# Kernel optimization log

Hardware: AMD Instinct MI355X
Metric: run time of the kernel (lower is better)

The kernel has to match this reference:

```python
import jax, jax.numpy as jnp
import numpy as np

N = 32768
NIN = 12
NC = 16
HID = 512
K = 8
B = 3.0
L = 8
D_HALF = NIN // 2                      # 6
DIN = D_HALF + NC                      # conditioner input
DOUT = (3 * K - 1) * (NIN - D_HALF)    # conditioner output
MIN_W = 1e-3
MIN_H = 1e-3
MIN_D = 1e-3
DERIV_CONST = float(np.log(np.exp(1.0 - MIN_D) - 1.0))  # softplus^{-1}(1-min_d)


def setup_inputs() -> dict:
    key = jax.random.key(0)
    ks = jax.random.split(key, 12)
    z = jax.random.normal(ks[0], (N, NIN), dtype=jnp.float32)
    c = jax.random.normal(ks[1], (N, NC), dtype=jnp.float32)

    def lin(k, fan_in, shape):
        bound = 1.0 / np.sqrt(fan_in)
        return jax.random.uniform(k, shape, jnp.float32, -bound, bound)

    W0 = lin(ks[2], DIN, (L, DIN, HID)); b0 = lin(ks[3], DIN, (L, HID))
    W1 = lin(ks[4], HID, (L, HID, HID)); b1 = lin(ks[5], HID, (L, HID))
    W2 = lin(ks[6], HID, (L, HID, HID)); b2 = lin(ks[7], HID, (L, HID))
    W3 = lin(ks[8], HID, (L, HID, DOUT)); b3 = lin(ks[9], HID, (L, DOUT))

    rng = np.random.default_rng(0)
    perms = jnp.asarray(np.stack([rng.permutation(NIN) for _ in range(L - 1)]),
                        dtype=jnp.int32)  # [L-1, NIN]
    return dict(z=z, c=c, W0=W0, b0=b0, W1=W1, b1=b1, W2=W2, b2=b2,
                W3=W3, b3=b3, perms=perms)


def _rqs(x, uw, uh, ud):
    """Unconstrained rational-quadratic spline (forward).
    x: [N, d2]; uw/uh: [N, d2, K]; ud: [N, d2, K+1] (already edge-padded)."""
    widths = jax.nn.softmax(uw, axis=-1)
    widths = MIN_W + (1.0 - MIN_W * K) * widths
    cw = jnp.cumsum(widths, axis=-1)
    cw = jnp.concatenate([jnp.zeros_like(cw[..., :1]), cw], axis=-1)
    cw = 2.0 * B * cw - B
    cw = cw.at[..., 0].set(-B).at[..., -1].set(B)
    w = cw[..., 1:] - cw[..., :-1]

    heights = jax.nn.softmax(uh, axis=-1)
    heights = MIN_H + (1.0 - MIN_H * K) * heights
    ch = jnp.cumsum(heights, axis=-1)
    ch = jnp.concatenate([jnp.zeros_like(ch[..., :1]), ch], axis=-1)
    ch = 2.0 * B * ch - B
    ch = ch.at[..., 0].set(-B).at[..., -1].set(B)
    h = ch[..., 1:] - ch[..., :-1]

    d = MIN_D + jax.nn.softplus(ud)  # [N, d2, K+1]

    xc = jnp.clip(x, -B, B)  # tails are handled by mask below
    # searchsorted: eps added only to the last knot for the search itself
    cw_search = cw.at[..., -1].add(1e-6)
    idx = jnp.clip(jnp.sum((xc[..., None] >= cw_search).astype(jnp.int32),
                           axis=-1) - 1, 0, K - 1)  # [N, d2]

    def g(a):
        return jnp.take_along_axis(a, idx[..., None], axis=-1)[..., 0]

    icw, iw = g(cw), g(w)
    ich, ih = g(ch), g(h)
    idelta = g(h / w)
    id0 = g(d)
    id1 = g(d[..., 1:])

    theta = (xc - icw) / iw
    t1m = theta * (1.0 - theta)
    num = ih * (idelta * theta**2 + id0 * t1m)
    den = idelta + (id0 + id1 - 2.0 * idelta) * t1m
    out = ich + num / den
    dnum = idelta**2 * (id1 * theta**2 + 2.0 * idelta * t1m
                        + id0 * (1.0 - theta)**2)
    lad = jnp.log(dnum) - 2.0 * jnp.log(den)

    inside = (x >= -B) & (x <= B)
    return jnp.where(inside, out, x), jnp.where(inside, lad, 0.0)


def _flow(z, c, W0, b0, W1, b1, W2, b2, W3, b3, perms):
    x = z
    total_ld = jnp.zeros(z.shape[0], dtype=z.dtype)
    for i in range(L):
        x1, x2 = x[:, :D_HALF], x[:, D_HALF:]
        inp = jnp.concatenate([x1, c], axis=-1)
        h0 = jax.nn.elu(inp @ W0[i] + b0[i])
        h1 = jax.nn.elu(h0 @ W1[i] + b1[i])
        h2 = jax.nn.elu(h1 @ W2[i] + b2[i])
        out = (h2 @ W3[i] + b3[i]).reshape(-1, NIN - D_HALF, 3 * K - 1)
        uw, uh, ud = out[..., :K], out[..., K:2 * K], out[..., 2 * K:]
        ud = jnp.pad(ud, ((0, 0), (0, 0), (1, 1)),
                     constant_values=DERIV_CONST)
        x2n, ld = _rqs(x2, uw, uh, ud)
        total_ld = total_ld + jnp.sum(ld, axis=-1)
        x = jnp.concatenate([x1, x2n], axis=-1)
        if i < L - 1:
            x = x[:, perms[i]]
    return x, total_ld


def reference(z, c, W0, b0, W1, b1, W2, b2, W3, b3, perms):
    return _flow(z, c, W0, b0, W1, b1, W2, b2, W3, b3, perms)
```

## Files before the change

### kernel.cpp

```cpp
#include <hip/hip_runtime.h>
#include <hip/hip_fp16.h>

#define NROWS   32768
#define MT      64
#define NTH     512
#define HS      520
#define OS      148
#define BND     3.0f

typedef _Float16 half_t;
typedef __attribute__((ext_vector_type(8))) _Float16 f16x8;
typedef __attribute__((ext_vector_type(4))) _Float16 f16x4;
typedef __attribute__((ext_vector_type(4))) float    f32x4;


__global__ void pack_frag(const float* __restrict__ src, half_t* __restrict__ dst,
                          int K, int Nn, int NT, int KS) {
  int l = blockIdx.z;
  int frag = blockIdx.x * 4 + (threadIdx.x >> 6);
  int lane = threadIdx.x & 63;
  int NF = NT * KS;
  if (frag >= NF) return;
  int nt = frag / KS, ks = frag - nt * KS;
  int n = nt * 16 + (lane & 15);
  int kb = ks * 32 + (lane >> 4) * 8;
  f16x8 v;
#pragma unroll
  for (int e = 0; e < 8; e++) {
    int k = kb + e;
    v[e] = (k < K && n < Nn) ? (half_t)src[((size_t)l * K + k) * Nn + n] : (half_t)0.f;
  }
  *(f16x8*)(dst + ((size_t)l * NF + frag) * 512 + lane * 8) = v;
}

__device__ __forceinline__ float elu_f(float v) {
  return v > 0.f ? v : (__expf(v) - 1.f);
}

__device__ __forceinline__ void gemm_elu(
    const half_t* A, int as, int ksteps,
    const half_t* __restrict__ Wf, int KSW,
    const float* __restrict__ bias,
    half_t* dst,
    int w, int lane, int lm, int lk) {
  f32x4 acc[4][4];
#pragma unroll
  for (int i = 0; i < 4; i++)
#pragma unroll
    for (int j = 0; j < 4; j++) acc[i][j] = (f32x4){0.f, 0.f, 0.f, 0.f};

  f16x8 a[2][4], b[4][4];
#pragma unroll
  for (int s = 0; s < 4; s++)
    if (s < ksteps) {
#pragma unroll
      for (int nt = 0; nt < 4; nt++)
        b[s][nt] = *(const f16x8*)(Wf + ((size_t)((w * 4 + nt) * KSW + s)) * 512 + lane * 8);
    }
#pragma unroll
  for (int s = 0; s < 2; s++)
    if (s < ksteps) {
      int ko = s * 32 + lk * 8;
#pragma unroll
      for (int mf = 0; mf < 4; mf++)
        a[s][mf] = *(const f16x8*)(A + (mf * 16 + lm) * as + ko);
    }
#pragma unroll
  for (int ks = 0; ks < ksteps; ks++) {
    const int bs = ks & 3, asx = ks & 1;
#pragma unroll
    for (int nt = 0; nt < 4; nt++)
#pragma unroll
      for (int mf = 0; mf < 4; mf++)
        acc[mf][nt] = __builtin_amdgcn_mfma_f32_16x16x32_f16(b[bs][nt], a[asx][mf], acc[mf][nt], 0, 0, 0);
    if (ks + 4 < ksteps) {
#pragma unroll
      for (int nt = 0; nt < 4; nt++)
        b[bs][nt] = *(const f16x8*)(Wf + ((size_t)((w * 4 + nt) * KSW + ks + 4)) * 512 + lane * 8);
    }
    if (ks + 2 < ksteps) {
      int ko = (ks + 2) * 32 + lk * 8;
#pragma unroll
      for (int mf = 0; mf < 4; mf++)
        a[asx][mf] = *(const f16x8*)(A + (mf * 16 + lm) * as + ko);
    }
  }
#pragma unroll
  for (int nt = 0; nt < 4; nt++) {
    int n0 = w * 64 + nt * 16 + lk * 4;
    f32x4 bv = *(const f32x4*)(bias + n0);
#pragma unroll
    for (int mf = 0; mf < 4; mf++) {
      f16x4 pv;
#pragma unroll
      for (int r = 0; r < 4; r++) pv[r] = (half_t)elu_f(acc[mf][nt][r] + bv[r]);
      *(f16x4*)(dst + (mf * 16 + lm) * HS + n0) = pv;
    }
  }
}

__device__ __forceinline__ void gemm_out(
    const half_t* A,
    const half_t* __restrict__ Wf,
    const float* __restrict__ bias,
    float* outb,
    int w, int lane, int lm, int lk) {
  f32x4 acc[4][2];
#pragma unroll
  for (int i = 0; i < 4; i++)
#pragma unroll
    for (int j = 0; j < 2; j++) acc[i][j] = (f32x4){0.f, 0.f, 0.f, 0.f};
  const bool has2 = (w == 0);

  f16x8 a[2][4], b[4][2];
#pragma unroll
  for (int s = 0; s < 4; s++) {
    b[s][0] = *(const f16x8*)(Wf + ((size_t)(w * 16 + s)) * 512 + lane * 8);
    if (has2) b[s][1] = *(const f16x8*)(Wf + ((size_t)(8 * 16 + s)) * 512 + lane * 8);
  }
#pragma unroll
  for (int s = 0; s < 2; s++) {
    int ko = s * 32 + lk * 8;
#pragma unroll
    for (int mf = 0; mf < 4; mf++)
      a[s][mf] = *(const f16x8*)(A + (mf * 16 + lm) * HS + ko);
  }
#pragma unroll
  for (int ks = 0; ks < 16; ks++) {
    const int bs = ks & 3, asx = ks & 1;
#pragma unroll
    for (int mf = 0; mf < 4; mf++)
      acc[mf][0] = __builtin_amdgcn_mfma_f32_16x16x32_f16(b[bs][0], a[asx][mf], acc[mf][0], 0, 0, 0);
    if (has2)
#pragma unroll
      for (int mf = 0; mf < 4; mf++)
        acc[mf][1] = __builtin_amdgcn_mfma_f32_16x16x32_f16(b[bs][1], a[asx][mf], acc[mf][1], 0, 0, 0);
    if (ks + 4 < 16) {
      b[bs][0] = *(const f16x8*)(Wf + ((size_t)(w * 16 + ks + 4)) * 512 + lane * 8);
      if (has2) b[bs][1] = *(const f16x8*)(Wf + ((size_t)(8 * 16 + ks + 4)) * 512 + lane * 8);
    }
    if (ks + 2 < 16) {
      int ko = (ks + 2) * 32 + lk * 8;
#pragma unroll
      for (int mf = 0; mf < 4; mf++)
        a[asx][mf] = *(const f16x8*)(A + (mf * 16 + lm) * HS + ko);
    }
  }
  {
    int n0 = w * 16 + lk * 4;
    f32x4 bv = *(const f32x4*)(bias + n0);
#pragma unroll
    for (int mf = 0; mf < 4; mf++) {
      f32x4 ov = acc[mf][0] + bv;
      *(f32x4*)(outb + (mf * 16 + lm) * OS + n0) = ov;
    }
  }
  if (has2) {
    int n0 = 128 + lk * 4;
    f32x4 bv;
#pragma unroll
    for (int r = 0; r < 4; r++) bv[r] = (n0 + r < 138) ? bias[n0 + r] : 0.f;
#pragma unroll
    for (int mf = 0; mf < 4; mf++) {
      f32x4 ov = acc[mf][1] + bv;
      *(f32x4*)(outb + (mf * 16 + lm) * OS + n0) = ov;
    }
  }
}

__global__ __launch_bounds__(NTH, 2) __attribute__((amdgpu_waves_per_eu(2, 2)))
void flow_kernel(const float* __restrict__ z, const float* __restrict__ c,
                 const float* __restrict__ b0, const float* __restrict__ b1,
                 const float* __restrict__ b2, const float* __restrict__ b3,
                 const int* __restrict__ perms,
                 const half_t* __restrict__ W0F, const half_t* __restrict__ W1F,
                 const half_t* __restrict__ W2F, const half_t* __restrict__ W3F,
                 float* __restrict__ out) {
  __shared__ half_t hbufA[MT * HS];
  __shared__ __align__(16) char smemB[MT * HS * 2];
  __shared__ half_t inpb[MT * 40];
  __shared__ half_t cbuf[MT * 16];
  __shared__ float xbuf[MT][12];
  __shared__ float ldpart[MT][6];
  __shared__ float ldtot[MT];
  __shared__ int   permbuf[7][12];

  half_t* hbufB  = (half_t*)smemB;
  float*  outbuf = (float*)smemB;

  int tid = threadIdx.x;
  int w = tid >> 6, lane = tid & 63;
  int lm = lane & 15, lk = lane >> 4;
  int row0 = blockIdx.x * MT;

  for (int it = tid; it < MT * 12; it += NTH) xbuf[it / 12][it % 12] = z[(size_t)row0 * 12 + it];
  for (int it = tid; it < MT * 16; it += NTH) cbuf[it] = (half_t)c[(size_t)row0 * 16 + it];
  for (int it = tid; it < 84; it += NTH) permbuf[it / 12][it % 12] = perms[it];
  if (tid < MT) ldtot[tid] = 0.f;
  __syncthreads();

  for (int l = 0; l < 8; l++) {
    for (int it = tid; it < MT * 32; it += NTH) {
      int m = it >> 5, k = it & 31;
      half_t bv;
      if (k < 6)       bv = (half_t)xbuf[m][k];
      else if (k < 22) bv = cbuf[m * 16 + (k - 6)];
      else             bv = (half_t)0.f;
      inpb[m * 40 + k] = bv;
    }
    __syncthreads();
    gemm_elu(inpb, 40, 1,  W0F + (size_t)l * 32 * 512,      1,  b0 + l * 512, hbufA, w, lane, lm, lk);
    __syncthreads();
    gemm_elu(hbufA, HS, 16, W1F + (size_t)l * 512 * 512,   16,  b1 + l * 512, hbufB, w, lane, lm, lk);
    __syncthreads();
    gemm_elu(hbufB, HS, 16, W2F + (size_t)l * 512 * 512,   16,  b2 + l * 512, hbufA, w, lane, lm, lk);
    __syncthreads();
    gemm_out(hbufA, W3F + (size_t)l * 144 * 512, b3 + l * 138, outbuf, w, lane, lm, lk);
    __syncthreads();

    if (tid < MT * 6) {
      int m = tid / 6, j = tid % 6;
      const float* pr = outbuf + m * OS + j * 23;
      float uw[8], uh[8], dd[9];
#pragma unroll
      for (int i = 0; i < 8; i++) uw[i] = pr[i];
#pragma unroll
      for (int i = 0; i < 8; i++) uh[i] = pr[8 + i];
      dd[0] = 1.f; dd[8] = 1.f;
#pragma unroll
      for (int i = 0; i < 7; i++) {
        float u = pr[16 + i];
        float sp = (u > 15.f) ? u : log1pf(__expf(u));
        dd[i + 1] = 0.001f + sp;
      }
      float mw = uw[0];
#pragma unroll
      for (int i = 1; i < 8; i++) mw = fmaxf(mw, uw[i]);
      float ew[8], sw = 0.f;
#pragma unroll
      for (int i = 0; i < 8; i++) { ew[i] = __expf(uw[i] - mw); sw += ew[i]; }
      float invw = 1.f / sw;
      float cw[9]; cw[0] = -BND;
      float a = 0.f;
#pragma unroll
      for (int i = 0; i < 8; i++) { a += 0.001f + 0.992f * ew[i] * invw; cw[i + 1] = 2.f * BND * a - BND; }
      cw[8] = BND;
      float mh = uh[0];
#pragma unroll
      for (int i = 1; i < 8; i++) mh = fmaxf(mh, uh[i]);
      float eh[8], sh = 0.f;
#pragma unroll
      for (int i = 0; i < 8; i++) { eh[i] = __expf(uh[i] - mh); sh += eh[i]; }
      float invh = 1.f / sh;
      float ch[9]; ch[0] = -BND;
      float ah = 0.f;
#pragma unroll
      for (int i = 0; i < 8; i++) { ah += 0.001f + 0.992f * eh[i] * invh; ch[i + 1] = 2.f * BND * ah - BND; }
      ch[8] = BND;

      float x2 = xbuf[m][6 + j];
      float xc = fminf(fmaxf(x2, -BND), BND);
      int cnt = 0;
#pragma unroll
      for (int i = 0; i < 9; i++) {
        float edge = (i == 8) ? (cw[8] + 1e-6f) : cw[i];
        cnt += (xc >= edge) ? 1 : 0;
      }
      int idx = cnt - 1; idx = idx < 0 ? 0 : (idx > 7 ? 7 : idx);
      float icw = cw[0], iw = cw[1] - cw[0], ich = ch[0], ih = ch[1] - ch[0], d0 = dd[0], d1 = dd[1];
#pragma unroll
      for (int i = 0; i < 8; i++) {
        if (idx == i) {
          icw = cw[i]; iw = cw[i + 1] - cw[i];
          ich = ch[i]; ih = ch[i + 1] - ch[i];
          d0 = dd[i]; d1 = dd[i + 1];
        }
      }
      float delta = ih / iw;
      float th  = (xc - icw) / iw;
      float t1m = th * (1.f - th);
      float num = ih * (delta * th * th + d0 * t1m);
      float den = delta + (d0 + d1 - 2.f * delta) * t1m;
      float outv = ich + num / den;
      float dnum = delta * delta * (d1 * th * th + 2.f * delta * t1m + d0 * (1.f - th) * (1.f - th));
      float lad = logf(dnum) - 2.f * logf(den);
      bool inside = (x2 >= -BND) && (x2 <= BND);
      xbuf[m][6 + j] = inside ? outv : x2;
      ldpart[m][j]   = inside ? lad : 0.f;
    }
    __syncthreads();
    if (tid < MT) {
      float s = ldtot[tid];
#pragma unroll
      for (int j = 0; j < 6; j++) s += ldpart[tid][j];
      ldtot[tid] = s;
    }
    if (l < 7) {
      float v0 = xbuf[tid / 12][permbuf[l][tid % 12]];
      float v1 = 0.f;
      int it1 = tid + NTH;
      if (it1 < MT * 12) v1 = xbuf[it1 / 12][permbuf[l][it1 % 12]];
      __syncthreads();
      xbuf[tid / 12][tid % 12] = v0;
      if (it1 < MT * 12) xbuf[it1 / 12][it1 % 12] = v1;
    }
    __syncthreads();
  }

  for (int it = tid; it < MT * 12; it += NTH) out[(size_t)row0 * 12 + it] = xbuf[it / 12][it % 12];
  if (tid < MT) out[(size_t)NROWS * 12 + row0 + tid] = ldtot[tid];
}

extern "C" void kernel_launch(void* const* d_in, const int* in_sizes, int n_in,
                              void* d_out, int out_size, void* d_ws, size_t ws_size,
                              hipStream_t stream) {
  const float* z  = (const float*)d_in[0];
  const float* c  = (const float*)d_in[1];
  const float* W0 = (const float*)d_in[2];
  const float* b0 = (const float*)d_in[3];
  const float* W1 = (const float*)d_in[4];
  const float* b1 = (const float*)d_in[5];
  const float* W2 = (const float*)d_in[6];
  const float* b2 = (const float*)d_in[7];
  const float* W3 = (const float*)d_in[8];
  const float* b3 = (const float*)d_in[9];
  const int* perms = (const int*)d_in[10];

  unsigned short* wsu = (unsigned short*)d_ws;
  half_t* W0F = (half_t*)(wsu + 0);
  half_t* W1F = (half_t*)(wsu + 131072);
  half_t* W2F = (half_t*)(wsu + 2228224);
  half_t* W3F = (half_t*)(wsu + 4325376);

  pack_frag<<<dim3(8,   1, 8), dim3(256), 0, stream>>>(W0, W0F, 22,  512, 32, 1);
  pack_frag<<<dim3(128, 1, 8), dim3(256), 0, stream>>>(W1, W1F, 512, 512, 32, 16);
  pack_frag<<<dim3(128, 1, 8), dim3(256), 0, stream>>>(W2, W2F, 512, 512, 32, 16);
  pack_frag<<<dim3(36,  1, 8), dim3(256), 0, stream>>>(W3, W3F, 512, 138, 9,  16);

  flow_kernel<<<dim3(NROWS / MT), dim3(NTH), 0, stream>>>(
      z, c, b0, b1, b2, b3, perms, W0F, W1F, W2F, W3F, (float*)d_out);
}
```

Before: 547.8 us.

## Prefetch next GEMM's first weight fragments across layer boundaries via register rings

```diff
diff --git a/kernel.cpp b/kernel.cpp
--- a/kernel.cpp
+++ b/kernel.cpp
@@ -37,54 +37,9 @@
   return v > 0.f ? v : (__expf(v) - 1.f);
 }
 
-__device__ __forceinline__ void gemm_elu(
-    const half_t* A, int as, int ksteps,
-    const half_t* __restrict__ Wf, int KSW,
-    const float* __restrict__ bias,
-    half_t* dst,
-    int w, int lane, int lm, int lk) {
-  f32x4 acc[4][4];
-#pragma unroll
-  for (int i = 0; i < 4; i++)
-#pragma unroll
-    for (int j = 0; j < 4; j++) acc[i][j] = (f32x4){0.f, 0.f, 0.f, 0.f};
-
-  f16x8 a[2][4], b[4][4];
-#pragma unroll
-  for (int s = 0; s < 4; s++)
-    if (s < ksteps) {
-#pragma unroll
-      for (int nt = 0; nt < 4; nt++)
-        b[s][nt] = *(const f16x8*)(Wf + ((size_t)((w * 4 + nt) * KSW + s)) * 512 + lane * 8);
-    }
-#pragma unroll
-  for (int s = 0; s < 2; s++)
-    if (s < ksteps) {
-      int ko = s * 32 + lk * 8;
-#pragma unroll
-      for (int mf = 0; mf < 4; mf++)
-        a[s][mf] = *(const f16x8*)(A + (mf * 16 + lm) * as + ko);
-    }
-#pragma unroll
-  for (int ks = 0; ks < ksteps; ks++) {
-    const int bs = ks & 3, asx = ks & 1;
-#pragma unroll
-    for (int nt = 0; nt < 4; nt++)
-#pragma unroll
-      for (int mf = 0; mf < 4; mf++)
-        acc[mf][nt] = __builtin_amdgcn_mfma_f32_16x16x32_f16(b[bs][nt], a[asx][mf], acc[mf][nt], 0, 0, 0);
-    if (ks + 4 < ksteps) {
-#pragma unroll
-      for (int nt = 0; nt < 4; nt++)
-        b[bs][nt] = *(const f16x8*)(Wf + ((size_t)((w * 4 + nt) * KSW + ks + 4)) * 512 + lane * 8);
-    }
-    if (ks + 2 < ksteps) {
-      int ko = (ks + 2) * 32 + lk * 8;
-#pragma unroll
-      for (int mf = 0; mf < 4; mf++)
-        a[asx][mf] = *(const f16x8*)(A + (mf * 16 + lm) * as + ko);
-    }
-  }
+__device__ __forceinline__ void epi_elu(const f32x4 (&acc)[4][4],
+                                        const float* __restrict__ bias,
+                                        half_t* dst, int w, int lm, int lk) {
 #pragma unroll
   for (int nt = 0; nt < 4; nt++) {
     int n0 = w * 64 + nt * 16 + lk * 4;
@@ -99,11 +54,86 @@
   }
 }
 
+__device__ __forceinline__ void gemm0(const half_t* A, const f16x8 (&b0r)[4],
+                                      const float* __restrict__ bias,
+                                      half_t* dst, int w, int lm, int lk) {
+  f32x4 acc[4][4];
+#pragma unroll
+  for (int i = 0; i < 4; i++)
+#pragma unroll
+    for (int j = 0; j < 4; j++) acc[i][j] = (f32x4){0.f, 0.f, 0.f, 0.f};
+  int ko = lk * 8;
+  f16x8 a[4];
+#pragma unroll
+  for (int mf = 0; mf < 4; mf++) a[mf] = *(const f16x8*)(A + (mf * 16 + lm) * 40 + ko);
+#pragma unroll
+  for (int nt = 0; nt < 4; nt++)
+#pragma unroll
+    for (int mf = 0; mf < 4; mf++)
+      acc[mf][nt] = __builtin_amdgcn_mfma_f32_16x16x32_f16(b0r[nt], a[mf], acc[mf][nt], 0, 0, 0);
+  epi_elu(acc, bias, dst, w, lm, lk);
+}
+
+template <bool FILL4>
+__device__ __forceinline__ void gemm512(
+    const half_t* A, const half_t* __restrict__ Wf,
+    const float* __restrict__ bias, half_t* dst,
+    f16x8 (&ring4)[4][4], f16x8 (&ring2)[4][2],
+    const half_t* __restrict__ nxt,
+    int w, int lane, int lm, int lk) {
+  f32x4 acc[4][4];
+#pragma unroll
+  for (int i = 0; i < 4; i++)
+#pragma unroll
+    for (int j = 0; j < 4; j++) acc[i][j] = (f32x4){0.f, 0.f, 0.f, 0.f};
+
+  f16x8 a[2][4];
+#pragma unroll
+  for (int s = 0; s < 2; s++) {
+    int ko = s * 32 + lk * 8;
+#pragma unroll
+    for (int mf = 0; mf < 4; mf++)
+      a[s][mf] = *(const f16x8*)(A + (mf * 16 + lm) * HS + ko);
+  }
+#pragma unroll
+  for (int ks = 0; ks < 16; ks++) {
+    const int sl = ks & 3, asx = ks & 1;
+#pragma unroll
+    for (int nt = 0; nt < 4; nt++)
+#pragma unroll
+      for (int mf = 0; mf < 4; mf++)
+        acc[mf][nt] = __builtin_amdgcn_mfma_f32_16x16x32_f16(ring4[sl][nt], a[asx][mf], acc[mf][nt], 0, 0, 0);
+    if (ks + 4 < 16) {
+#pragma unroll
+      for (int nt = 0; nt < 4; nt++)
+        ring4[sl][nt] = *(const f16x8*)(Wf + ((size_t)((w * 4 + nt) * 16 + ks + 4)) * 512 + lane * 8);
+    } else {
+      int j = ks - 12;
+      if (FILL4) {
+#pragma unroll
+        for (int nt = 0; nt < 4; nt++)
+          ring4[sl][nt] = *(const f16x8*)(nxt + ((size_t)((w * 4 + nt) * 16 + j)) * 512 + lane * 8);
+      } else {
+        ring2[sl][0] = *(const f16x8*)(nxt + ((size_t)(w * 16 + j)) * 512 + lane * 8);
+        if (w == 0)
+          ring2[sl][1] = *(const f16x8*)(nxt + ((size_t)(128 + j)) * 512 + lane * 8);
+      }
+    }
+    if (ks + 2 < 16) {
+      int ko = (ks + 2) * 32 + lk * 8;
+#pragma unroll
+      for (int mf = 0; mf < 4; mf++)
+        a[asx][mf] = *(const f16x8*)(A + (mf * 16 + lm) * HS + ko);
+    }
+  }
+  epi_elu(acc, bias, dst, w, lm, lk);
+}
+
 __device__ __forceinline__ void gemm_out(
-    const half_t* A,
-    const half_t* __restrict__ Wf,
-    const float* __restrict__ bias,
-    float* outb,
+    const half_t* A, const half_t* __restrict__ Wf,
+    const float* __restrict__ bias, float* outb,
+    f16x8 (&ring2)[4][2], f16x8 (&ring4)[4][4],
+    const half_t* __restrict__ nxtW1,
     int w, int lane, int lm, int lk) {
   f32x4 acc[4][2];
 #pragma unroll
@@ -112,12 +142,7 @@
     for (int j = 0; j < 2; j++) acc[i][j] = (f32x4){0.f, 0.f, 0.f, 0.f};
   const bool has2 = (w == 0);
 
-  f16x8 a[2][4], b[4][2];
-#pragma unroll
-  for (int s = 0; s < 4; s++) {
-    b[s][0] = *(const f16x8*)(Wf + ((size_t)(w * 16 + s)) * 512 + lane * 8);
-    if (has2) b[s][1] = *(const f16x8*)(Wf + ((size_t)(8 * 16 + s)) * 512 + lane * 8);
-  }
+  f16x8 a[2][4];
 #pragma unroll
   for (int s = 0; s < 2; s++) {
     int ko = s * 32 + lk * 8;
@@ -127,17 +152,22 @@
   }
 #pragma unroll
   for (int ks = 0; ks < 16; ks++) {
-    const int bs = ks & 3, asx = ks & 1;
+    const int sl = ks & 3, asx = ks & 1;
 #pragma unroll
     for (int mf = 0; mf < 4; mf++)
-      acc[mf][0] = __builtin_amdgcn_mfma_f32_16x16x32_f16(b[bs][0], a[asx][mf], acc[mf][0], 0, 0, 0);
+      acc[mf][0] = __builtin_amdgcn_mfma_f32_16x16x32_f16(ring2[sl][0], a[asx][mf], acc[mf][0], 0, 0, 0);
     if (has2)
 #pragma unroll
       for (int mf = 0; mf < 4; mf++)
-        acc[mf][1] = __builtin_amdgcn_mfma_f32_16x16x32_f16(b[bs][1], a[asx][mf], acc[mf][1], 0, 0, 0);
+        acc[mf][1] = __builtin_amdgcn_mfma_f32_16x16x32_f16(ring2[sl][1], a[asx][mf], acc[mf][1], 0, 0, 0);
     if (ks + 4 < 16) {
-      b[bs][0] = *(const f16x8*)(Wf + ((size_t)(w * 16 + ks + 4)) * 512 + lane * 8);
-      if (has2) b[bs][1] = *(const f16x8*)(Wf + ((size_t)(8 * 16 + ks + 4)) * 512 + lane * 8);
+      ring2[sl][0] = *(const f16x8*)(Wf + ((size_t)(w * 16 + ks + 4)) * 512 + lane * 8);
+      if (has2) ring2[sl][1] = *(const f16x8*)(Wf + ((size_t)(128 + ks + 4)) * 512 + lane * 8);
+    } else {
+      int j = ks - 12;
+#pragma unroll
+      for (int nt = 0; nt < 4; nt++)
+        ring4[sl][nt] = *(const f16x8*)(nxtW1 + ((size_t)((w * 4 + nt) * 16 + j)) * 512 + lane * 8);
     }
     if (ks + 2 < 16) {
       int ko = (ks + 2) * 32 + lk * 8;
@@ -193,6 +223,13 @@
   int lm = lane & 15, lk = lane >> 4;
   int row0 = blockIdx.x * MT;
 
+  f16x8 ring4[4][4], ring2[4][2];
+#pragma unroll
+  for (int s = 0; s < 4; s++)
+#pragma unroll
+    for (int nt = 0; nt < 4; nt++)
+      ring4[s][nt] = *(const f16x8*)(W1F + ((size_t)((w * 4 + nt) * 16 + s)) * 512 + lane * 8);
+
   for (int it = tid; it < MT * 12; it += NTH) xbuf[it / 12][it % 12] = z[(size_t)row0 * 12 + it];
   for (int it = tid; it < MT * 16; it += NTH) cbuf[it] = (half_t)c[(size_t)row0 * 16 + it];
   for (int it = tid; it < 84; it += NTH) permbuf[it / 12][it % 12] = perms[it];
@@ -200,6 +237,13 @@
   __syncthreads();
 
   for (int l = 0; l < 8; l++) {
+    f16x8 b0r[4];
+    {
+      const half_t* W0l = W0F + (size_t)l * 32 * 512;
+#pragma unroll
+      for (int nt = 0; nt < 4; nt++)
+        b0r[nt] = *(const f16x8*)(W0l + ((size_t)(w * 4 + nt)) * 512 + lane * 8);
+    }
     for (int it = tid; it < MT * 32; it += NTH) {
       int m = it >> 5, k = it & 31;
       half_t bv;
@@ -209,13 +253,17 @@
       inpb[m * 40 + k] = bv;
     }
     __syncthreads();
-    gemm_elu(inpb, 40, 1,  W0F + (size_t)l * 32 * 512,      1,  b0 + l * 512, hbufA, w, lane, lm, lk);
-    __syncthreads();
-    gemm_elu(hbufA, HS, 16, W1F + (size_t)l * 512 * 512,   16,  b1 + l * 512, hbufB, w, lane, lm, lk);
-    __syncthreads();
-    gemm_elu(hbufB, HS, 16, W2F + (size_t)l * 512 * 512,   16,  b2 + l * 512, hbufA, w, lane, lm, lk);
-    __syncthreads();
-    gemm_out(hbufA, W3F + (size_t)l * 144 * 512, b3 + l * 138, outbuf, w, lane, lm, lk);
+
+    gemm0(inpb, b0r, b0 + l * 512, hbufA, w, lm, lk);
+    __syncthreads();
+    gemm512<true >(hbufA, W1F + (size_t)l * 512 * 512, b1 + l * 512, hbufB,
+                   ring4, ring2, W2F + (size_t)l * 512 * 512, w, lane, lm, lk);
+    __syncthreads();
+    gemm512<false>(hbufB, W2F + (size_t)l * 512 * 512, b2 + l * 512, hbufA,
+                   ring4, ring2, W3F + (size_t)l * 144 * 512, w, lane, lm, lk);
+    __syncthreads();
+    gemm_out(hbufA, W3F + (size_t)l * 144 * 512, b3 + l * 138, outbuf,
+             ring2, ring4, W1F + (size_t)((l + 1) & 7) * 512 * 512, w, lane, lm, lk);
     __syncthreads();
 
     if (tid < MT * 6) {
```

After: 570.0 us. 4.1% more time.

## Double block to 16 waves and split GEMM N-tiles across more waves

Applied to the files above, without the earlier changes.

```diff
diff --git a/kernel.cpp b/kernel.cpp
--- a/kernel.cpp
+++ b/kernel.cpp
@@ -3,7 +3,7 @@
 
 #define NROWS   32768
 #define MT      64
-#define NTH     512
+#define NTH     1024
 #define HS      520
 #define OS      148
 #define BND     3.0f
@@ -37,57 +37,12 @@
   return v > 0.f ? v : (__expf(v) - 1.f);
 }
 
-__device__ __forceinline__ void gemm_elu(
-    const half_t* A, int as, int ksteps,
-    const half_t* __restrict__ Wf, int KSW,
-    const float* __restrict__ bias,
-    half_t* dst,
-    int w, int lane, int lm, int lk) {
-  f32x4 acc[4][4];
-#pragma unroll
-  for (int i = 0; i < 4; i++)
-#pragma unroll
-    for (int j = 0; j < 4; j++) acc[i][j] = (f32x4){0.f, 0.f, 0.f, 0.f};
-
-  f16x8 a[2][4], b[4][4];
-#pragma unroll
-  for (int s = 0; s < 4; s++)
-    if (s < ksteps) {
-#pragma unroll
-      for (int nt = 0; nt < 4; nt++)
-        b[s][nt] = *(const f16x8*)(Wf + ((size_t)((w * 4 + nt) * KSW + s)) * 512 + lane * 8);
-    }
-#pragma unroll
-  for (int s = 0; s < 2; s++)
-    if (s < ksteps) {
-      int ko = s * 32 + lk * 8;
-#pragma unroll
-      for (int mf = 0; mf < 4; mf++)
-        a[s][mf] = *(const f16x8*)(A + (mf * 16 + lm) * as + ko);
-    }
-#pragma unroll
-  for (int ks = 0; ks < ksteps; ks++) {
-    const int bs = ks & 3, asx = ks & 1;
-#pragma unroll
-    for (int nt = 0; nt < 4; nt++)
-#pragma unroll
-      for (int mf = 0; mf < 4; mf++)
-        acc[mf][nt] = __builtin_amdgcn_mfma_f32_16x16x32_f16(b[bs][nt], a[asx][mf], acc[mf][nt], 0, 0, 0);
-    if (ks + 4 < ksteps) {
-#pragma unroll
-      for (int nt = 0; nt < 4; nt++)
-        b[bs][nt] = *(const f16x8*)(Wf + ((size_t)((w * 4 + nt) * KSW + ks + 4)) * 512 + lane * 8);
-    }
-    if (ks + 2 < ksteps) {
-      int ko = (ks + 2) * 32 + lk * 8;
-#pragma unroll
-      for (int mf = 0; mf < 4; mf++)
-        a[asx][mf] = *(const f16x8*)(A + (mf * 16 + lm) * as + ko);
-    }
-  }
-#pragma unroll
-  for (int nt = 0; nt < 4; nt++) {
-    int n0 = w * 64 + nt * 16 + lk * 4;
+__device__ __forceinline__ void epi_elu(const f32x4 (&acc)[4][2],
+                                        const float* __restrict__ bias,
+                                        half_t* dst, int w, int lm, int lk) {
+#pragma unroll
+  for (int nt = 0; nt < 2; nt++) {
+    int n0 = w * 32 + nt * 16 + lk * 4;
     f32x4 bv = *(const f32x4*)(bias + n0);
 #pragma unroll
     for (int mf = 0; mf < 4; mf++) {
@@ -99,25 +54,47 @@
   }
 }
 
-__device__ __forceinline__ void gemm_out(
-    const half_t* A,
-    const half_t* __restrict__ Wf,
-    const float* __restrict__ bias,
-    float* outb,
+__device__ __forceinline__ void gemm0(const half_t* A,
+                                      const half_t* __restrict__ Wf,
+                                      const float* __restrict__ bias,
+                                      half_t* dst, int w, int lane, int lm, int lk) {
+  f32x4 acc[4][2];
+#pragma unroll
+  for (int i = 0; i < 4; i++)
+#pragma unroll
+    for (int j = 0; j < 2; j++) acc[i][j] = (f32x4){0.f, 0.f, 0.f, 0.f};
+  f16x8 b[2];
+#pragma unroll
+  for (int nt = 0; nt < 2; nt++)
+    b[nt] = *(const f16x8*)(Wf + ((size_t)(w * 2 + nt)) * 512 + lane * 8);
+  int ko = lk * 8;
+  f16x8 a[4];
+#pragma unroll
+  for (int mf = 0; mf < 4; mf++) a[mf] = *(const f16x8*)(A + (mf * 16 + lm) * 40 + ko);
+#pragma unroll
+  for (int nt = 0; nt < 2; nt++)
+#pragma unroll
+    for (int mf = 0; mf < 4; mf++)
+      acc[mf][nt] = __builtin_amdgcn_mfma_f32_16x16x32_f16(b[nt], a[mf], acc[mf][nt], 0, 0, 0);
+  epi_elu(acc, bias, dst, w, lm, lk);
+}
+
+__device__ __forceinline__ void gemm512(
+    const half_t* A, const half_t* __restrict__ Wf,
+    const float* __restrict__ bias, half_t* dst,
     int w, int lane, int lm, int lk) {
   f32x4 acc[4][2];
 #pragma unroll
   for (int i = 0; i < 4; i++)
 #pragma unroll
     for (int j = 0; j < 2; j++) acc[i][j] = (f32x4){0.f, 0.f, 0.f, 0.f};
-  const bool has2 = (w == 0);
 
   f16x8 a[2][4], b[4][2];
 #pragma unroll
-  for (int s = 0; s < 4; s++) {
-    b[s][0] = *(const f16x8*)(Wf + ((size_t)(w * 16 + s)) * 512 + lane * 8);
-    if (has2) b[s][1] = *(const f16x8*)(Wf + ((size_t)(8 * 16 + s)) * 512 + lane * 8);
-  }
+  for (int s = 0; s < 4; s++)
+#pragma unroll
+    for (int nt = 0; nt < 2; nt++)
+      b[s][nt] = *(const f16x8*)(Wf + ((size_t)((w * 2 + nt) * 16 + s)) * 512 + lane * 8);
 #pragma unroll
   for (int s = 0; s < 2; s++) {
     int ko = s * 32 + lk * 8;
@@ -127,17 +104,16 @@
   }
 #pragma unroll
   for (int ks = 0; ks < 16; ks++) {
-    const int bs = ks & 3, asx = ks & 1;
-#pragma unroll
-    for (int mf = 0; mf < 4; mf++)
-      acc[mf][0] = __builtin_amdgcn_mfma_f32_16x16x32_f16(b[bs][0], a[asx][mf], acc[mf][0], 0, 0, 0);
-    if (has2)
+    const int sl = ks & 3, asx = ks & 1;
+#pragma unroll
+    for (int nt = 0; nt < 2; nt++)
 #pragma unroll
       for (int mf = 0; mf < 4; mf++)
-        acc[mf][1] = __builtin_amdgcn_mfma_f32_16x16x32_f16(b[bs][1], a[asx][mf], acc[mf][1], 0, 0, 0);
+        acc[mf][nt] = __builtin_amdgcn_mfma_f32_16x16x32_f16(b[sl][nt], a[asx][mf], acc[mf][nt], 0, 0, 0);
     if (ks + 4 < 16) {
-      b[bs][0] = *(const f16x8*)(Wf + ((size_t)(w * 16 + ks + 4)) * 512 + lane * 8);
-      if (has2) b[bs][1] = *(const f16x8*)(Wf + ((size_t)(8 * 16 + ks + 4)) * 512 + lane * 8);
+#pragma unroll
+      for (int nt = 0; nt < 2; nt++)
+        b[sl][nt] = *(const f16x8*)(Wf + ((size_t)((w * 2 + nt) * 16 + ks + 4)) * 512 + lane * 8);
     }
     if (ks + 2 < 16) {
       int ko = (ks + 2) * 32 + lk * 8;
@@ -146,29 +122,56 @@
         a[asx][mf] = *(const f16x8*)(A + (mf * 16 + lm) * HS + ko);
     }
   }
-  {
-    int n0 = w * 16 + lk * 4;
-    f32x4 bv = *(const f32x4*)(bias + n0);
-#pragma unroll
-    for (int mf = 0; mf < 4; mf++) {
-      f32x4 ov = acc[mf][0] + bv;
-      *(f32x4*)(outb + (mf * 16 + lm) * OS + n0) = ov;
-    }
-  }
-  if (has2) {
-    int n0 = 128 + lk * 4;
-    f32x4 bv;
-#pragma unroll
-    for (int r = 0; r < 4; r++) bv[r] = (n0 + r < 138) ? bias[n0 + r] : 0.f;
-#pragma unroll
-    for (int mf = 0; mf < 4; mf++) {
-      f32x4 ov = acc[mf][1] + bv;
-      *(f32x4*)(outb + (mf * 16 + lm) * OS + n0) = ov;
-    }
-  }
-}
-
-__global__ __launch_bounds__(NTH, 2) __attribute__((amdgpu_waves_per_eu(2, 2)))
+  epi_elu(acc, bias, dst, w, lm, lk);
+}
+
+__device__ __forceinline__ void gemm_out(
+    const half_t* A, const half_t* __restrict__ Wf,
+    const float* __restrict__ bias,
+    float* outb, int w, int lane, int lm, int lk) {
+  if (w >= 9) return;
+  f32x4 acc[4];
+#pragma unroll
+  for (int i = 0; i < 4; i++) acc[i] = (f32x4){0.f, 0.f, 0.f, 0.f};
+
+  f16x8 a[2][4], b[4];
+#pragma unroll
+  for (int s = 0; s < 4; s++)
+    b[s] = *(const f16x8*)(Wf + ((size_t)(w * 16 + s)) * 512 + lane * 8);
+#pragma unroll
+  for (int s = 0; s < 2; s++) {
+    int ko = s * 32 + lk * 8;
+#pragma unroll
+    for (int mf = 0; mf < 4; mf++)
+      a[s][mf] = *(const f16x8*)(A + (mf * 16 + lm) * HS + ko);
+  }
+#pragma unroll
+  for (int ks = 0; ks < 16; ks++) {
+    const int sl = ks & 3, asx = ks & 1;
+#pragma unroll
+    for (int mf = 0; mf < 4; mf++)
+      acc[mf] = __builtin_amdgcn_mfma_f32_16x16x32_f16(b[sl], a[asx][mf], acc[mf], 0, 0, 0);
+    if (ks + 4 < 16)
+      b[sl] = *(const f16x8*)(Wf + ((size_t)(w * 16 + ks + 4)) * 512 + lane * 8);
+    if (ks + 2 < 16) {
+      int ko = (ks + 2) * 32 + lk * 8;
+#pragma unroll
+      for (int mf = 0; mf < 4; mf++)
+        a[asx][mf] = *(const f16x8*)(A + (mf * 16 + lm) * HS + ko);
+    }
+  }
+  int n0 = w * 16 + lk * 4;
+  f32x4 bv;
+#pragma unroll
+  for (int r = 0; r < 4; r++) bv[r] = (n0 + r < 138) ? bias[n0 + r] : 0.f;
+#pragma unroll
+  for (int mf = 0; mf < 4; mf++) {
+    f32x4 ov = acc[mf] + bv;
+    *(f32x4*)(outb + (mf * 16 + lm) * OS + n0) = ov;
+  }
+}
+
+__global__ __launch_bounds__(NTH, 4) __attribute__((amdgpu_waves_per_eu(4, 4)))
 void flow_kernel(const float* __restrict__ z, const float* __restrict__ c,
                  const float* __restrict__ b0, const float* __restrict__ b1,
                  const float* __restrict__ b2, const float* __restrict__ b3,
@@ -193,9 +196,9 @@
   int lm = lane & 15, lk = lane >> 4;
   int row0 = blockIdx.x * MT;
 
-  for (int it = tid; it < MT * 12; it += NTH) xbuf[it / 12][it % 12] = z[(size_t)row0 * 12 + it];
-  for (int it = tid; it < MT * 16; it += NTH) cbuf[it] = (half_t)c[(size_t)row0 * 16 + it];
-  for (int it = tid; it < 84; it += NTH) permbuf[it / 12][it % 12] = perms[it];
+  if (tid < MT * 12) xbuf[tid / 12][tid % 12] = z[(size_t)row0 * 12 + tid];
+  if (tid < MT * 16) cbuf[tid] = (half_t)c[(size_t)row0 * 16 + tid];
+  if (tid < 84) permbuf[tid / 12][tid % 12] = perms[tid];
   if (tid < MT) ldtot[tid] = 0.f;
   __syncthreads();
 
@@ -209,11 +212,11 @@
       inpb[m * 40 + k] = bv;
     }
     __syncthreads();
-    gemm_elu(inpb, 40, 1,  W0F + (size_t)l * 32 * 512,      1,  b0 + l * 512, hbufA, w, lane, lm, lk);
-    __syncthreads();
-    gemm_elu(hbufA, HS, 16, W1F + (size_t)l * 512 * 512,   16,  b1 + l * 512, hbufB, w, lane, lm, lk);
-    __syncthreads();
-    gemm_elu(hbufB, HS, 16, W2F + (size_t)l * 512 * 512,   16,  b2 + l * 512, hbufA, w, lane, lm, lk);
+    gemm0(inpb, W0F + (size_t)l * 32 * 512, b0 + l * 512, hbufA, w, lane, lm, lk);
+    __syncthreads();
+    gemm512(hbufA, W1F + (size_t)l * 512 * 512, b1 + l * 512, hbufB, w, lane, lm, lk);
+    __syncthreads();
+    gemm512(hbufB, W2F + (size_t)l * 512 * 512, b2 + l * 512, hbufA, w, lane, lm, lk);
     __syncthreads();
     gemm_out(hbufA, W3F + (size_t)l * 144 * 512, b3 + l * 138, outbuf, w, lane, lm, lk);
     __syncthreads();
@@ -296,18 +299,15 @@
       ldtot[tid] = s;
     }
     if (l < 7) {
-      float v0 = xbuf[tid / 12][permbuf[l][tid % 12]];
-      float v1 = 0.f;
-      int it1 = tid + NTH;
-      if (it1 < MT * 12) v1 = xbuf[it1 / 12][permbuf[l][it1 % 12]];
+      float v0 = 0.f;
+      if (tid < MT * 12) v0 = xbuf[tid / 12][permbuf[l][tid % 12]];
       __syncthreads();
-      xbuf[tid / 12][tid % 12] = v0;
-      if (it1 < MT * 12) xbuf[it1 / 12][it1 % 12] = v1;
-    }
-    __syncthreads();
-  }
-
-  for (int it = tid; it < MT * 12; it += NTH) out[(size_t)row0 * 12 + it] = xbuf[it / 12][it % 12];
+      if (tid < MT * 12) xbuf[tid / 12][tid % 12] = v0;
+    }
+    __syncthreads();
+  }
+
+  if (tid < MT * 12) out[(size_t)row0 * 12 + tid] = xbuf[tid / 12][tid % 12];
   if (tid < MT) out[(size_t)NROWS * 12 + row0 + tid] = ldtot[tid];
 }
 
```

Measured after the change: 626.3 us. 14.3% more time.
